# Kernel optimization log

Measured on AMD Instinct MI355X. Metric: run time of the kernel, lower is better.

The kernel has to match this reference:

```python
import jax, jax.numpy as jnp
import numpy as np

TEMPERATURE = 8.0      # sqrt(d_head=64), matches init temperature
MASK_FILL = -1e32      # masked_softmax memory_efficient fill value
B, L, D = 16, 2048, 64


def setup_inputs() -> dict:
    key = jax.random.key(0)
    kq, kk, kv, kd, km = jax.random.split(key, 5)
    q = jax.random.normal(kq, (B, L, D), dtype=jnp.float32)
    k = jax.random.normal(kk, (B, L, D), dtype=jnp.float32)
    v = jax.random.normal(kv, (B, L, D), dtype=jnp.float32)
    diag_mask = jax.random.randint(kd, (B, L, L), 0, 2, dtype=jnp.int32)  # 1=keep, 0=mask
    mask = jax.random.randint(km, (B, L, L), 0, 2, dtype=jnp.int32).astype(jnp.bool_)  # True=mask out
    return {"q": q, "k": k, "v": v, "diag_mask": diag_mask, "mask": mask}


def reference(q, k, v, diag_mask, mask):
    # attn = q @ k^T / temperature   -> [B, Lq, Lk]
    attn = jnp.einsum('bqd,bkd->bqk', q, k) / TEMPERATURE
    # attn.masked_fill(mask, -inf)
    attn = jnp.where(mask, -jnp.inf, attn)
    # masked_softmax(attn, diag_mask, memory_efficient=True):
    #   masked_fill((1 - diag_mask).bool(), -1e32) then softmax
    attn = jnp.where(diag_mask == 0, MASK_FILL, attn)
    attn = jax.nn.softmax(attn, axis=-1)
    # output = attn @ v
    output = jnp.einsum('bqk,bkd->bqd', attn, v)
    return output, attn
```

## Files before the change

kernel.cpp:

```cpp
#include <hip/hip_runtime.h>
#include <math.h>

#define NB 16
#define SL 2048
#define HD 64
#define TQ 16
#define BK 64
#define NT (SL / BK)
#define SCALE 0.125f
#define SSTRIDE 2056

typedef _Float16 half8 __attribute__((ext_vector_type(8)));
typedef float floatx4 __attribute__((ext_vector_type(4)));
typedef int intx4 __attribute__((ext_vector_type(4)));

__device__ __forceinline__ half8 load_frag_f32(const float* p) {
  floatx4 f0 = *(const floatx4*)p;
  floatx4 f1 = *(const floatx4*)(p + 4);
  half8 h;
  h[0] = (_Float16)f0[0]; h[1] = (_Float16)f0[1];
  h[2] = (_Float16)f0[2]; h[3] = (_Float16)f0[3];
  h[4] = (_Float16)f1[0]; h[5] = (_Float16)f1[1];
  h[6] = (_Float16)f1[2]; h[7] = (_Float16)f1[3];
  return h;
}

__global__ __launch_bounds__(512) void attn_kernel(
    const float* __restrict__ Q, const float* __restrict__ K,
    const float* __restrict__ V, const int* __restrict__ DM,
    const int* __restrict__ MMk, float* __restrict__ Out,
    float* __restrict__ Attn)
{
  const int qt    = blockIdx.x;
  const int b     = blockIdx.y;
  const int tid   = (int)threadIdx.x;
  const int w     = tid >> 6;
  const int w4    = w & 3;
  const int hf    = w >> 2;
  const int lane  = tid & 63;
  const int quad  = lane >> 4;
  const int nl    = lane & 15;
  const int row16 = tid >> 5;
  const int ci    = tid & 31;

  const int qbase    = qt * TQ;
  const size_t bLD   = (size_t)b * SL * HD;
  const size_t mbase = ((size_t)b * SL + qbase) * SL;

  __shared__ __align__(16) _Float16 S[TQ * SSTRIDE];
  __shared__ float sinv_s[TQ];
  __shared__ float obuf[TQ][65];

  half8 aq0, aq1;
  {
    const float* qp = Q + bLD + (size_t)(qbase + nl) * HD + quad * 8;
    aq0 = load_frag_f32(qp);
    aq1 = load_frag_f32(qp + 32);
  }

  const int kt0 = hf * (NT / 2);
  #pragma unroll 2
  for (int kti = 0; kti < NT / 2; ++kti) {
    const int kt = kt0 + kti;
    const float* kp = K + bLD + (size_t)(kt * BK + w4 * 16 + nl) * HD + quad * 8;
    half8 bk0 = load_frag_f32(kp);
    half8 bk1 = load_frag_f32(kp + 32);
    floatx4 acc = {0.f, 0.f, 0.f, 0.f};
    acc = __builtin_amdgcn_mfma_f32_16x16x32_f16(aq0, bk0, acc, 0, 0, 0);
    acc = __builtin_amdgcn_mfma_f32_16x16x32_f16(aq1, bk1, acc, 0, 0, 0);
    const int col = kt * BK + w4 * 16 + nl;
    #pragma unroll
    for (int r = 0; r < 4; ++r)
      S[(quad * 4 + r) * SSTRIDE + col] = (_Float16)(acc[r] * SCALE);
  }
  __syncthreads();

  const int* dmr = DM  + mbase + (size_t)row16 * SL;
  const int* mkr = MMk + mbase + (size_t)row16 * SL;
  _Float16* srow = &S[row16 * SSTRIDE];

  float sum = 0.f;
  #pragma unroll 4
  for (int it = 0; it < 8; ++it) {
    const int c = it * 256 + ci * 8;
    intx4 d0 = __builtin_nontemporal_load((const intx4*)(dmr + c));
    intx4 d1 = __builtin_nontemporal_load((const intx4*)(dmr + c + 4));
    intx4 m0 = __builtin_nontemporal_load((const intx4*)(mkr + c));
    intx4 m1 = __builtin_nontemporal_load((const intx4*)(mkr + c + 4));
    half8 s8 = *(const half8*)(srow + c);
    half8 e8;
    #pragma unroll
    for (int j = 0; j < 4; ++j) {
      const bool k0 = (d0[j] != 0) && (m0[j] == 0);
      const bool k1 = (d1[j] != 0) && (m1[j] == 0);
      const float e0 = k0 ? __expf((float)s8[j])     : 0.f;
      const float e1 = k1 ? __expf((float)s8[j + 4]) : 0.f;
      sum += e0 + e1;
      e8[j]     = (_Float16)e0;
      e8[j + 4] = (_Float16)e1;
    }
    *(half8*)(srow + c) = e8;
  }
  #pragma unroll
  for (int off = 1; off < 32; off <<= 1)
    sum += __shfl_xor(sum, off, 64);
  const float is = (sum > 0.f) ? 1.f / sum : 0.f;
  if (ci == 0) sinv_s[row16] = is;

  float* arow = Attn + mbase + (size_t)row16 * SL;
  #pragma unroll 4
  for (int it = 0; it < 8; ++it) {
    const int c = it * 256 + ci * 8;
    half8 e8 = *(const half8*)(srow + c);
    floatx4 o0, o1;
    #pragma unroll
    for (int j = 0; j < 4; ++j) {
      o0[j] = (float)e8[j]     * is;
      o1[j] = (float)e8[j + 4] * is;
    }
    __builtin_nontemporal_store(o0, (floatx4*)(arow + c));
    __builtin_nontemporal_store(o1, (floatx4*)(arow + c + 4));
  }
  __syncthreads();

  floatx4 oacc = {0.f, 0.f, 0.f, 0.f};
  #pragma unroll 2
  for (int kti = 0; kti < NT / 2; ++kti) {
    const int kt = kt0 + kti;
    half8 ap0 = *(const half8*)(&S[nl * SSTRIDE + kt * BK + quad * 8]);
    half8 ap1 = *(const half8*)(&S[nl * SSTRIDE + kt * BK + quad * 8 + 32]);
    half8 bv0, bv1;
    const float* vp = V + bLD + (size_t)(kt * BK + quad * 8) * HD + w4 * 16 + nl;
    #pragma unroll
    for (int j = 0; j < 8; ++j) {
      bv0[j] = (_Float16)vp[(size_t)j * HD];
      bv1[j] = (_Float16)vp[(size_t)(j + 32) * HD];
    }
    oacc = __builtin_amdgcn_mfma_f32_16x16x32_f16(ap0, bv0, oacc, 0, 0, 0);
    oacc = __builtin_amdgcn_mfma_f32_16x16x32_f16(ap1, bv1, oacc, 0, 0, 0);
  }

  if (hf == 1) {
    #pragma unroll
    for (int r = 0; r < 4; ++r)
      obuf[quad * 4 + r][w4 * 16 + nl] = oacc[r];
  }
  __syncthreads();
  if (hf == 0) {
    float* op = Out + ((size_t)b * SL + qbase) * HD;
    #pragma unroll
    for (int r = 0; r < 4; ++r) {
      const int row = quad * 4 + r;
      op[(size_t)row * HD + w4 * 16 + nl] =
          (oacc[r] + obuf[row][w4 * 16 + nl]) * sinv_s[row];
    }
  }
}

extern "C" void kernel_launch(void* const* d_in, const int* in_sizes, int n_in,
                              void* d_out, int out_size, void* d_ws, size_t ws_size,
                              hipStream_t stream) {
  const float* Q  = (const float*)d_in[0];
  const float* K  = (const float*)d_in[1];
  const float* V  = (const float*)d_in[2];
  const int* DM   = (const int*)d_in[3];
  const int* MMk  = (const int*)d_in[4];
  float* Out  = (float*)d_out;
  float* Attn = (float*)d_out + (size_t)NB * SL * HD;
  dim3 grid(SL / TQ, NB);
  attn_kernel<<<grid, 512, 0, stream>>>(Q, K, V, DM, MMk, Out, Attn);
}
```

Measured before the change: 740.6 us.

## Prefetch masks early, pre-convert K/V to fp16, interleave attn stores with PV

Adds a prep kernel that converts K to fp16 and V to a transposed fp16 layout in workspace, so the main kernel can load MFMA fragments with vector loads instead of strided fp32 gathers. Mask and diag_mask loads are issued into registers before the QK^T phase to hide their latency, and the scale is folded into a log2e factor so exp2 replaces expf. Attention probability stores are interleaved into the PV MFMA loop after a barrier. The cost is higher register pressure from 32 prefetched int vectors and an extra kernel launch plus workspace traffic; the prep path only runs if the workspace is large enough.

```diff
diff --git a/kernel.cpp b/kernel.cpp
--- a/kernel.cpp
+++ b/kernel.cpp
@@ -7,7 +7,7 @@
 #define TQ 16
 #define BK 64
 #define NT (SL / BK)
-#define SCALE 0.125f
+#define SC2 0.18033688f
 #define SSTRIDE 2056
 
 typedef _Float16 half8 __attribute__((ext_vector_type(8)));
@@ -25,9 +25,49 @@
   return h;
 }
 
+__global__ __launch_bounds__(256) void prep_kernel(
+    const float* __restrict__ K, const float* __restrict__ V,
+    _Float16* __restrict__ KH, _Float16* __restrict__ VT)
+{
+  __shared__ __align__(16) _Float16 tile[64][72];
+  const int t  = (int)threadIdx.x;
+  const int k0 = blockIdx.x * 64;
+  const int b  = blockIdx.y;
+  const size_t base = (size_t)b * SL * HD;
+  const int r  = t >> 2;
+  const int cq = (t & 3) * 16;
+
+  const float* kp = K + base + (size_t)(k0 + r) * HD + cq;
+  const float* vp = V + base + (size_t)(k0 + r) * HD + cq;
+  half8 kh0 = load_frag_f32(kp), kh1 = load_frag_f32(kp + 8);
+  half8 vh0 = load_frag_f32(vp), vh1 = load_frag_f32(vp + 8);
+
+  _Float16* khp = KH + base + (size_t)(k0 + r) * HD + cq;
+  *(half8*)khp       = kh0;
+  *(half8*)(khp + 8) = kh1;
+
+  const int wc = cq ^ (((r >> 4) & 3) * 16);
+  *(half8*)&tile[r][wc]     = vh0;
+  *(half8*)&tile[r][wc + 8] = vh1;
+  __syncthreads();
+
+  const int sx = ((cq >> 4) & 3) * 16;
+  half8 o0, o1;
+  #pragma unroll
+  for (int i = 0; i < 8; ++i) {
+    o0[i] = tile[cq + i][r ^ sx];
+    o1[i] = tile[cq + 8 + i][r ^ sx];
+  }
+  _Float16* vt = VT + (size_t)b * HD * SL + (size_t)r * SL + k0 + cq;
+  *(half8*)vt       = o0;
+  *(half8*)(vt + 8) = o1;
+}
+
+template <bool PREP>
 __global__ __launch_bounds__(512) void attn_kernel(
     const float* __restrict__ Q, const float* __restrict__ K,
-    const float* __restrict__ V, const int* __restrict__ DM,
+    const float* __restrict__ V, const _Float16* __restrict__ KH,
+    const _Float16* __restrict__ VT, const int* __restrict__ DM,
     const int* __restrict__ MMk, float* __restrict__ Out,
     float* __restrict__ Attn)
 {
@@ -51,6 +91,18 @@
   __shared__ float sinv_s[TQ];
   __shared__ float obuf[TQ][65];
 
+  const int* dmr = DM  + mbase + (size_t)row16 * SL;
+  const int* mkr = MMk + mbase + (size_t)row16 * SL;
+  intx4 pd0[8], pd1[8], pm0[8], pm1[8];
+  #pragma unroll
+  for (int it = 0; it < 8; ++it) {
+    const int c = it * 256 + ci * 8;
+    pd0[it] = __builtin_nontemporal_load((const intx4*)(dmr + c));
+    pd1[it] = __builtin_nontemporal_load((const intx4*)(dmr + c + 4));
+    pm0[it] = __builtin_nontemporal_load((const intx4*)(mkr + c));
+    pm1[it] = __builtin_nontemporal_load((const intx4*)(mkr + c + 4));
+  }
+
   half8 aq0, aq1;
   {
     const float* qp = Q + bLD + (size_t)(qbase + nl) * HD + quad * 8;
@@ -62,39 +114,39 @@
   #pragma unroll 2
   for (int kti = 0; kti < NT / 2; ++kti) {
     const int kt = kt0 + kti;
-    const float* kp = K + bLD + (size_t)(kt * BK + w4 * 16 + nl) * HD + quad * 8;
-    half8 bk0 = load_frag_f32(kp);
-    half8 bk1 = load_frag_f32(kp + 32);
+    half8 bk0, bk1;
+    if constexpr (PREP) {
+      const _Float16* kp = KH + bLD + (size_t)(kt * BK + w4 * 16 + nl) * HD + quad * 8;
+      bk0 = *(const half8*)kp;
+      bk1 = *(const half8*)(kp + 32);
+    } else {
+      const float* kp = K + bLD + (size_t)(kt * BK + w4 * 16 + nl) * HD + quad * 8;
+      bk0 = load_frag_f32(kp);
+      bk1 = load_frag_f32(kp + 32);
+    }
     floatx4 acc = {0.f, 0.f, 0.f, 0.f};
     acc = __builtin_amdgcn_mfma_f32_16x16x32_f16(aq0, bk0, acc, 0, 0, 0);
     acc = __builtin_amdgcn_mfma_f32_16x16x32_f16(aq1, bk1, acc, 0, 0, 0);
     const int col = kt * BK + w4 * 16 + nl;
     #pragma unroll
     for (int r = 0; r < 4; ++r)
-      S[(quad * 4 + r) * SSTRIDE + col] = (_Float16)(acc[r] * SCALE);
-  }
-  __syncthreads();
-
-  const int* dmr = DM  + mbase + (size_t)row16 * SL;
-  const int* mkr = MMk + mbase + (size_t)row16 * SL;
+      S[(quad * 4 + r) * SSTRIDE + col] = (_Float16)(acc[r] * SC2);
+  }
+  __syncthreads();
+
   _Float16* srow = &S[row16 * SSTRIDE];
-
   float sum = 0.f;
-  #pragma unroll 4
+  #pragma unroll
   for (int it = 0; it < 8; ++it) {
     const int c = it * 256 + ci * 8;
-    intx4 d0 = __builtin_nontemporal_load((const intx4*)(dmr + c));
-    intx4 d1 = __builtin_nontemporal_load((const intx4*)(dmr + c + 4));
-    intx4 m0 = __builtin_nontemporal_load((const intx4*)(mkr + c));
-    intx4 m1 = __builtin_nontemporal_load((const intx4*)(mkr + c + 4));
     half8 s8 = *(const half8*)(srow + c);
     half8 e8;
     #pragma unroll
     for (int j = 0; j < 4; ++j) {
-      const bool k0 = (d0[j] != 0) && (m0[j] == 0);
-      const bool k1 = (d1[j] != 0) && (m1[j] == 0);
-      const float e0 = k0 ? __expf((float)s8[j])     : 0.f;
-      const float e1 = k1 ? __expf((float)s8[j + 4]) : 0.f;
+      const int keep0 = pd0[it][j] & ~pm0[it][j];
+      const int keep1 = pd1[it][j] & ~pm1[it][j];
+      const float e0 = keep0 ? __builtin_amdgcn_exp2f((float)s8[j])     : 0.f;
+      const float e1 = keep1 ? __builtin_amdgcn_exp2f((float)s8[j + 4]) : 0.f;
       sum += e0 + e1;
       e8[j]     = (_Float16)e0;
       e8[j + 4] = (_Float16)e1;
@@ -106,38 +158,43 @@
     sum += __shfl_xor(sum, off, 64);
   const float is = (sum > 0.f) ? 1.f / sum : 0.f;
   if (ci == 0) sinv_s[row16] = is;
-
+  __syncthreads();
+
+  const float isr = sinv_s[row16];
   float* arow = Attn + mbase + (size_t)row16 * SL;
-  #pragma unroll 4
-  for (int it = 0; it < 8; ++it) {
-    const int c = it * 256 + ci * 8;
-    half8 e8 = *(const half8*)(srow + c);
-    floatx4 o0, o1;
-    #pragma unroll
-    for (int j = 0; j < 4; ++j) {
-      o0[j] = (float)e8[j]     * is;
-      o1[j] = (float)e8[j + 4] * is;
-    }
-    __builtin_nontemporal_store(o0, (floatx4*)(arow + c));
-    __builtin_nontemporal_store(o1, (floatx4*)(arow + c + 4));
-  }
-  __syncthreads();
-
   floatx4 oacc = {0.f, 0.f, 0.f, 0.f};
-  #pragma unroll 2
+  #pragma unroll
   for (int kti = 0; kti < NT / 2; ++kti) {
     const int kt = kt0 + kti;
     half8 ap0 = *(const half8*)(&S[nl * SSTRIDE + kt * BK + quad * 8]);
     half8 ap1 = *(const half8*)(&S[nl * SSTRIDE + kt * BK + quad * 8 + 32]);
     half8 bv0, bv1;
-    const float* vp = V + bLD + (size_t)(kt * BK + quad * 8) * HD + w4 * 16 + nl;
-    #pragma unroll
-    for (int j = 0; j < 8; ++j) {
-      bv0[j] = (_Float16)vp[(size_t)j * HD];
-      bv1[j] = (_Float16)vp[(size_t)(j + 32) * HD];
+    if constexpr (PREP) {
+      const _Float16* vp = VT + bLD + (size_t)(w4 * 16 + nl) * SL + kt * BK + quad * 8;
+      bv0 = *(const half8*)vp;
+      bv1 = *(const half8*)(vp + 32);
+    } else {
+      const float* vp = V + bLD + (size_t)(kt * BK + quad * 8) * HD + w4 * 16 + nl;
+      #pragma unroll
+      for (int j = 0; j < 8; ++j) {
+        bv0[j] = (_Float16)vp[(size_t)j * HD];
+        bv1[j] = (_Float16)vp[(size_t)(j + 32) * HD];
+      }
     }
     oacc = __builtin_amdgcn_mfma_f32_16x16x32_f16(ap0, bv0, oacc, 0, 0, 0);
     oacc = __builtin_amdgcn_mfma_f32_16x16x32_f16(ap1, bv1, oacc, 0, 0, 0);
+    if ((kti & 1) == 0) {
+      const int c = (kti >> 1) * 256 + ci * 8;
+      half8 e8v = *(const half8*)(srow + c);
+      floatx4 o0, o1;
+      #pragma unroll
+      for (int j = 0; j < 4; ++j) {
+        o0[j] = (float)e8v[j]     * isr;
+        o1[j] = (float)e8v[j + 4] * isr;
+      }
+      __builtin_nontemporal_store(o0, (floatx4*)(arow + c));
+      __builtin_nontemporal_store(o1, (floatx4*)(arow + c + 4));
+    }
   }
 
   if (hf == 1) {
@@ -168,5 +225,13 @@
   float* Out  = (float*)d_out;
   float* Attn = (float*)d_out + (size_t)NB * SL * HD;
   dim3 grid(SL / TQ, NB);
-  attn_kernel<<<grid, 512, 0, stream>>>(Q, K, V, DM, MMk, Out, Attn);
-}
+  const size_t need = (size_t)2 * NB * SL * HD * sizeof(_Float16);
+  if (d_ws != nullptr && ws_size >= need) {
+    _Float16* KH = (_Float16*)d_ws;
+    _Float16* VT = KH + (size_t)NB * SL * HD;
+    prep_kernel<<<dim3(SL / 64, NB), 256, 0, stream>>>(K, V, KH, VT);
+    attn_kernel<true><<<grid, 512, 0, stream>>>(Q, K, V, KH, VT, DM, MMk, Out, Attn);
+  } else {
+    attn_kernel<false><<<grid, 512, 0, stream>>>(Q, K, V, nullptr, nullptr, DM, MMk, Out, Attn);
+  }
+}
```

After: 727.7 us. About the same (-1.7%).
